# Optimization experiments

Hardware: AMD Instinct MI355X
Metric: run time of the kernel (lower is better)

Reference implementation:

```python
import jax, jax.numpy as jnp
import numpy as np

N = 50000   # nodes
E = 800000  # edges
F = 128     # feature dim per layer
BN_EPS = 1e-5


def setup_inputs() -> dict:
    key = jax.random.key(0)
    ks = jax.random.split(key, 4)
    x = jax.random.normal(ks[0], (N, F), dtype=jnp.float32)
    edge_index = jax.random.randint(ks[1], (2, E), 0, N, dtype=jnp.int64)
    scale = 1.0 / np.sqrt(F)
    W1 = jax.random.normal(ks[2], (F, F), dtype=jnp.float32) * scale
    W2 = jax.random.normal(ks[3], (F, F), dtype=jnp.float32) * scale
    zeros = jnp.zeros((F,), dtype=jnp.float32)
    ones = jnp.ones((F,), dtype=jnp.float32)
    prelu = jnp.full((1,), 0.25, dtype=jnp.float32)
    return {
        "x": x, "edge_index": edge_index,
        "W1": W1, "b1": zeros, "g1": ones, "be1": zeros, "a1": prelu,
        "W2": W2, "b2": zeros, "g2": ones, "be2": zeros, "a2": prelu,
    }


def _gcn_norm(edge_index):
    # PyG GCNConv: add self-loops, symmetric normalization D^-1/2 A D^-1/2
    src, dst = edge_index[0], edge_index[1]
    loop = jnp.arange(N, dtype=src.dtype)
    src_a = jnp.concatenate([src, loop])  # [E+N]
    dst_a = jnp.concatenate([dst, loop])
    w = jnp.ones((E + N,), dtype=jnp.float32)
    deg = jax.ops.segment_sum(w, dst_a, num_segments=N)
    dinv = jnp.where(deg > 0, jax.lax.rsqrt(jnp.maximum(deg, 1.0)), 0.0)
    norm = dinv[src_a] * w * dinv[dst_a]  # [E+N]
    return src_a, dst_a, norm


def _layer(x, src_a, dst_a, norm, W, b, g, be, a):
    h = x @ W                                    # [N,F] dense transform
    msg = h[src_a] * norm[:, None]               # gather [E+N,F]
    agg = jax.ops.segment_sum(msg, dst_a, num_segments=N) + b  # scatter-add
    # BatchNorm1d (training mode: biased batch statistics over nodes)
    mu = jnp.mean(agg, axis=0)
    var = jnp.mean(jnp.square(agg - mu), axis=0)
    xh = (agg - mu) * jax.lax.rsqrt(var + BN_EPS) * g + be
    # PReLU (single shared weight)
    return jnp.where(xh >= 0, xh, a * xh)


def reference(x, edge_index, W1, b1, g1, be1, a1, W2, b2, g2, be2, a2):
    src_a, dst_a, norm = _gcn_norm(edge_index)
    x = _layer(x, src_a, dst_a, norm, W1, b1, g1, be1, a1)
    x = _layer(x, src_a, dst_a, norm, W2, b2, g2, be2, a2)
    return x
```

## Files before the change

### kernel.cpp

```cpp
#include <hip/hip_runtime.h>

#define FD 128
#define BN_EPS 1e-5f
#define BSH 8
#define CAP 6144
#define BE 8192
#define NGB 2048
#define NRB 64

typedef short s8v __attribute__((ext_vector_type(8)));
typedef float f4v __attribute__((ext_vector_type(4)));

__device__ __forceinline__ unsigned short f2bf(float f) {
    unsigned u = __float_as_uint(f);
    u += 0x7fff + ((u >> 16) & 1);
    return (unsigned short)(u >> 16);
}
__device__ __forceinline__ float bf_lo(unsigned int u) {
    return __uint_as_float(u << 16);
}
__device__ __forceinline__ float bf_hi(unsigned int u) {
    return __uint_as_float(u & 0xffff0000u);
}

__global__ __launch_bounds__(256) void detect_kernel(const int* __restrict__ ei,
                                                     int n32, int* flag, int* gcur) {
    __shared__ int any;
    gcur[threadIdx.x] = 0;
    if (threadIdx.x == 0) any = 0;
    __syncthreads();
    int limit = n32 < 4096 ? n32 : 4096;
    int found = 0;
    for (int i = threadIdx.x * 2 + 1; i < limit; i += 512) {
        if (ei[i] != 0) { found = 1; break; }
    }
    if (found) atomicOr(&any, 1);
    __syncthreads();
    if (threadIdx.x == 0) flag[0] = any ? 0 : 1;
}

__device__ __forceinline__ int edge_get(const void* ei, int is64, size_t idx) {
    return is64 ? (int)((const long long*)ei)[idx] : ((const int*)ei)[idx];
}

__global__ __launch_bounds__(256) void partition_kernel(const void* ei, const int* flag,
                                                        int* __restrict__ gcur,
                                                        unsigned* __restrict__ slab, int E) {
    __shared__ int hist[256];
    __shared__ int base[256];
    __shared__ int cur[256];
    int t = threadIdx.x;
    int e0 = blockIdx.x * BE;
    int cnt = E - e0; if (cnt > BE) cnt = BE;
    hist[t] = 0;
    __syncthreads();
    int is64 = flag[0];
    for (int i = t; i < cnt; i += 256) {
        int d = edge_get(ei, is64, (size_t)E + e0 + i);
        atomicAdd(&hist[d >> BSH], 1);
    }
    __syncthreads();
    base[t] = hist[t] ? atomicAdd(&gcur[t], hist[t]) : 0;
    cur[t] = 0;
    __syncthreads();
    for (int i = t; i < cnt; i += 256) {
        int s = edge_get(ei, is64, e0 + i);
        int d = edge_get(ei, is64, (size_t)E + e0 + i);
        int b = d >> BSH;
        int r = atomicAdd(&cur[b], 1);
        int pos = base[b] + r;
        if (pos < CAP)
            slab[(size_t)b * CAP + pos] = (unsigned)s | ((unsigned)(d & 255) << 24);
    }
}

__global__ __launch_bounds__(256) void bucket_csr_kernel(const unsigned* __restrict__ slab,
                                                         const int* __restrict__ gcur,
                                                         int* __restrict__ colslab,
                                                         uint4* __restrict__ nodemeta,
                                                         float* __restrict__ dinv, int n) {
    __shared__ int hist[256];
    __shared__ int loc[256];
    __shared__ int cur[256];
    __shared__ int tmp[256];
    int b = blockIdx.x, t = threadIdx.x;
    hist[t] = 0;
    __syncthreads();
    int cnt = gcur[b]; if (cnt > CAP) cnt = CAP;
    const unsigned* sl = slab + (size_t)b * CAP;
    for (int i = t; i < cnt; i += 256)
        atomicAdd(&hist[sl[i] >> 24], 1);
    __syncthreads();
    int v = hist[t];
    tmp[t] = v;
    __syncthreads();
    for (int off = 1; off < 256; off <<= 1) {
        int x = (t >= off) ? tmp[t - off] : 0;
        __syncthreads();
        tmp[t] += x;
        __syncthreads();
    }
    int start_loc = tmp[t] - v;
    loc[t] = start_loc;
    cur[t] = 0;
    int node = (b << BSH) + t;
    if (node < n) {
        float dv = rsqrtf(1.0f + (float)v);
        dinv[node] = dv;
        nodemeta[node] = make_uint4((unsigned)(b * CAP + start_loc), (unsigned)v,
                                    __float_as_uint(dv), 0u);
    }
    __syncthreads();
    for (int i = t; i < cnt; i += 256) {
        unsigned e = sl[i];
        int dl = e >> 24;
        int r = atomicAdd(&cur[dl], 1);
        colslab[(size_t)b * CAP + loc[dl] + r] = (int)(e & 0xFFFFFF);
    }
}

__global__ __launch_bounds__(256) void wprep_kernel(const float* __restrict__ W1,
                                                    const float* __restrict__ W2,
                                                    unsigned short* __restrict__ Wf1,
                                                    unsigned short* __restrict__ Wf2) {
    int blk = blockIdx.x;
    const float* W = (blk < 64) ? W1 : W2;
    unsigned short* Wf = (blk < 64) ? Wf1 : Wf2;
    int idx = (blk & 63) * 256 + threadIdx.x;
    int j = idx & 7, lane = (idx >> 3) & 63, ct = (idx >> 9) & 7, kt = idx >> 12;
    int k = kt * 32 + (lane >> 4) * 8 + j;
    int c = ct * 16 + (lane & 15);
    Wf[idx] = f2bf(W[k * FD + c]);
}

template<int MODE>
__global__ __launch_bounds__(256) void gemm_mfma_kernel(const float* __restrict__ Ain,
                                                        const unsigned short* __restrict__ Wfrag,
                                                        const float* __restrict__ dinv,
                                                        const float4* __restrict__ scsh,
                                                        const float* __restrict__ aP,
                                                        unsigned short* __restrict__ C,
                                                        int n) {
    int wave = threadIdx.x >> 6, lane = threadIdx.x & 63;
    int rbase = blockIdx.x * 64 + wave * 16;
    int lrow = rbase + (lane & 15);
    int kg = lane >> 4;
    bool rok = lrow < n;
    float alpha = MODE ? aP[0] : 0.f;

    f4v acc[8];
#pragma unroll
    for (int i = 0; i < 8; ++i) acc[i] = (f4v){0.f, 0.f, 0.f, 0.f};

    const s8v* wf = (const s8v*)Wfrag;

#pragma unroll
    for (int kt = 0; kt < 4; ++kt) {
        s8v afr = (s8v){0, 0, 0, 0, 0, 0, 0, 0};
        if (rok) {
            const float* p = Ain + (size_t)lrow * FD + kt * 32 + kg * 8;
            float4 u0 = *(const float4*)p;
            float4 u1 = *(const float4*)(p + 4);
            if (MODE) {
                int c4 = kt * 8 + kg * 2;
                float4 sc0 = scsh[c4],      sh0 = scsh[32 + c4];
                float4 sc1 = scsh[c4 + 1],  sh1 = scsh[32 + c4 + 1];
                u0.x = u0.x * sc0.x + sh0.x; u0.y = u0.y * sc0.y + sh0.y;
                u0.z = u0.z * sc0.z + sh0.z; u0.w = u0.w * sc0.w + sh0.w;
                u1.x = u1.x * sc1.x + sh1.x; u1.y = u1.y * sc1.y + sh1.y;
                u1.z = u1.z * sc1.z + sh1.z; u1.w = u1.w * sc1.w + sh1.w;
                u0.x = u0.x >= 0.f ? u0.x : alpha * u0.x;
                u0.y = u0.y >= 0.f ? u0.y : alpha * u0.y;
                u0.z = u0.z >= 0.f ? u0.z : alpha * u0.z;
                u0.w = u0.w >= 0.f ? u0.w : alpha * u0.w;
                u1.x = u1.x >= 0.f ? u1.x : alpha * u1.x;
                u1.y = u1.y >= 0.f ? u1.y : alpha * u1.y;
                u1.z = u1.z >= 0.f ? u1.z : alpha * u1.z;
                u1.w = u1.w >= 0.f ? u1.w : alpha * u1.w;
            }
            afr[0] = (short)f2bf(u0.x); afr[1] = (short)f2bf(u0.y);
            afr[2] = (short)f2bf(u0.z); afr[3] = (short)f2bf(u0.w);
            afr[4] = (short)f2bf(u1.x); afr[5] = (short)f2bf(u1.y);
            afr[6] = (short)f2bf(u1.z); afr[7] = (short)f2bf(u1.w);
        }
#pragma unroll
        for (int ct = 0; ct < 8; ++ct) {
            s8v bfr = wf[(kt * 8 + ct) * 64 + lane];
            acc[ct] = __builtin_amdgcn_mfma_f32_16x16x32_bf16(afr, bfr, acc[ct], 0, 0, 0);
        }
    }

    int col0 = lane & 15;
#pragma unroll
    for (int r = 0; r < 4; ++r) {
        int row = rbase + kg * 4 + r;
        if (row < n) {
            float dv = dinv[row];
            unsigned short* crow = C + (size_t)row * FD;
#pragma unroll
            for (int ct = 0; ct < 8; ++ct)
                crow[ct * 16 + col0] = f2bf(acc[ct][r] * dv);
        }
    }
}

__global__ __launch_bounds__(256) void gather_stats_kernel(const uint2* __restrict__ hs2,
                                                           const uint4* __restrict__ nodemeta,
                                                           const int* __restrict__ col,
                                                           const float* __restrict__ b,
                                                           float4* __restrict__ agg4,
                                                           float4* __restrict__ partial,
                                                           int n) {
    __shared__ float4 redS[256];
    __shared__ float4 redQ[256];
    int tid = threadIdx.x;
    int hid = blockIdx.x * 8 + (tid >> 5);
    int q = tid & 31;
    float4 bb = ((const float4*)b)[q];

    float4 ssum = {0.f, 0.f, 0.f, 0.f};
    float4 ssq  = {0.f, 0.f, 0.f, 0.f};

    for (int wid = hid; wid < n; wid += NGB * 8) {
        uint4 m = nodemeta[wid];
        int i0 = (int)m.x, cnt = (int)m.y;
        float dv = __uint_as_float(m.z);
        uint2 u = hs2[(size_t)wid * 32 + q];
        float ax = bf_lo(u.x), ay = bf_hi(u.x), az = bf_lo(u.y), aw = bf_hi(u.y);
        int j = 0;
        for (; j + 4 <= cnt; j += 4) {
            int s0 = col[i0 + j], s1 = col[i0 + j + 1];
            int s2 = col[i0 + j + 2], s3 = col[i0 + j + 3];
            uint2 u0 = hs2[(size_t)s0 * 32 + q];
            uint2 u1 = hs2[(size_t)s1 * 32 + q];
            uint2 u2 = hs2[(size_t)s2 * 32 + q];
            uint2 u3 = hs2[(size_t)s3 * 32 + q];
            ax += bf_lo(u0.x) + bf_lo(u1.x) + bf_lo(u2.x) + bf_lo(u3.x);
            ay += bf_hi(u0.x) + bf_hi(u1.x) + bf_hi(u2.x) + bf_hi(u3.x);
            az += bf_lo(u0.y) + bf_lo(u1.y) + bf_lo(u2.y) + bf_lo(u3.y);
            aw += bf_hi(u0.y) + bf_hi(u1.y) + bf_hi(u2.y) + bf_hi(u3.y);
        }
        for (; j < cnt; ++j) {
            int s = col[i0 + j];
            uint2 uu = hs2[(size_t)s * 32 + q];
            ax += bf_lo(uu.x); ay += bf_hi(uu.x); az += bf_lo(uu.y); aw += bf_hi(uu.y);
        }
        float4 o;
        o.x = dv * ax + bb.x; o.y = dv * ay + bb.y;
        o.z = dv * az + bb.z; o.w = dv * aw + bb.w;
        agg4[(size_t)wid * 32 + q] = o;
        ssum.x += o.x; ssum.y += o.y; ssum.z += o.z; ssum.w += o.w;
        ssq.x += o.x * o.x; ssq.y += o.y * o.y;
        ssq.z += o.z * o.z; ssq.w += o.w * o.w;
    }
    redS[tid] = ssum;
    redQ[tid] = ssq;
    __syncthreads();
    if (tid < 128) {
        redS[tid].x += redS[tid+128].x; redS[tid].y += redS[tid+128].y;
        redS[tid].z += redS[tid+128].z; redS[tid].w += redS[tid+128].w;
        redQ[tid].x += redQ[tid+128].x; redQ[tid].y += redQ[tid+128].y;
        redQ[tid].z += redQ[tid+128].z; redQ[tid].w += redQ[tid+128].w;
    }
    __syncthreads();
    if (tid < 64) {
        redS[tid].x += redS[tid+64].x; redS[tid].y += redS[tid+64].y;
        redS[tid].z += redS[tid+64].z; redS[tid].w += redS[tid+64].w;
        redQ[tid].x += redQ[tid+64].x; redQ[tid].y += redQ[tid+64].y;
        redQ[tid].z += redQ[tid+64].z; redQ[tid].w += redQ[tid+64].w;
    }
    __syncthreads();
    if (tid < 32) {
        float4 s = redS[tid], s2 = redS[tid + 32];
        float4 qq = redQ[tid], q2 = redQ[tid + 32];
        s.x += s2.x; s.y += s2.y; s.z += s2.z; s.w += s2.w;
        qq.x += q2.x; qq.y += q2.y; qq.z += q2.z; qq.w += q2.w;
        partial[(size_t)blockIdx.x * 64 + tid] = s;
        partial[(size_t)blockIdx.x * 64 + 32 + tid] = qq;
    }
}

__global__ __launch_bounds__(256) void reduce_partial_kernel(const float4* __restrict__ partial,
                                                             float4* __restrict__ partial2) {
    __shared__ float4 red[256];
    int t = threadIdx.x;
    int e = t & 63;
    int sr = t >> 6;
    int r0 = blockIdx.x * 32;
    float4 acc = {0.f, 0.f, 0.f, 0.f};
    for (int r = sr; r < 32; r += 4) {
        float4 v = partial[(size_t)(r0 + r) * 64 + e];
        acc.x += v.x; acc.y += v.y; acc.z += v.z; acc.w += v.w;
    }
    red[t] = acc;
    __syncthreads();
    if (sr < 2) {
        float4 o = red[t + 128];
        red[t].x += o.x; red[t].y += o.y; red[t].z += o.z; red[t].w += o.w;
    }
    __syncthreads();
    if (sr == 0) {
        float4 o = red[t + 64];
        float4 s = red[t];
        s.x += o.x; s.y += o.y; s.z += o.z; s.w += o.w;
        partial2[(size_t)blockIdx.x * 64 + e] = s;
    }
}

__global__ __launch_bounds__(1024) void bn_finalize_kernel(const float4* __restrict__ partial2,
                                                           const float* __restrict__ g,
                                                           const float* __restrict__ be,
                                                           float4* __restrict__ scsh,
                                                           float invn) {
    __shared__ float4 red[1024];
    int t = threadIdx.x;
    int e = t & 63;
    int rg = t >> 6;
    float4 acc = {0.f, 0.f, 0.f, 0.f};
    for (int r = rg; r < NRB; r += 16) {
        float4 v = partial2[(size_t)r * 64 + e];
        acc.x += v.x; acc.y += v.y; acc.z += v.z; acc.w += v.w;
    }
    red[t] = acc;
    __syncthreads();
#pragma unroll
    for (int s = 8; s >= 1; s >>= 1) {
        if (rg < s) {
            float4 o = red[t + s * 64];
            red[t].x += o.x; red[t].y += o.y; red[t].z += o.z; red[t].w += o.w;
        }
        __syncthreads();
    }
    if (t < 32) {
        float4 s = red[t];
        float4 qq = red[32 + t];
        float4 gg = ((const float4*)g)[t];
        float4 bbe = ((const float4*)be)[t];
        float4 mu, var, sc, sh;
        mu.x = s.x * invn; mu.y = s.y * invn; mu.z = s.z * invn; mu.w = s.w * invn;
        var.x = qq.x * invn - mu.x * mu.x; var.y = qq.y * invn - mu.y * mu.y;
        var.z = qq.z * invn - mu.z * mu.z; var.w = qq.w * invn - mu.w * mu.w;
        sc.x = gg.x * rsqrtf(var.x + BN_EPS); sc.y = gg.y * rsqrtf(var.y + BN_EPS);
        sc.z = gg.z * rsqrtf(var.z + BN_EPS); sc.w = gg.w * rsqrtf(var.w + BN_EPS);
        sh.x = bbe.x - mu.x * sc.x; sh.y = bbe.y - mu.y * sc.y;
        sh.z = bbe.z - mu.z * sc.z; sh.w = bbe.w - mu.w * sc.w;
        scsh[t] = sc;
        scsh[32 + t] = sh;
    }
}

__global__ __launch_bounds__(256) void bn_apply_kernel(const float4* __restrict__ agg4,
                                                       const float4* __restrict__ scsh,
                                                       const float* __restrict__ aP,
                                                       float4* __restrict__ out, int n) {
    int t = blockIdx.x * 256 + threadIdx.x;
    if (t >= n * 32) return;
    int c4 = t & 31;
    float alpha = aP[0];
    float4 v = agg4[t];
    float4 sc = scsh[c4];
    float4 sh = scsh[32 + c4];
    float4 y;
    y.x = v.x * sc.x + sh.x; y.y = v.y * sc.y + sh.y;
    y.z = v.z * sc.z + sh.z; y.w = v.w * sc.w + sh.w;
    y.x = y.x >= 0.f ? y.x : alpha * y.x;
    y.y = y.y >= 0.f ? y.y : alpha * y.y;
    y.z = y.z >= 0.f ? y.z : alpha * y.z;
    y.w = y.w >= 0.f ? y.w : alpha * y.w;
    out[t] = y;
}


extern "C" void kernel_launch(void* const* d_in, const int* in_sizes, int n_in,
                              void* d_out, int out_size, void* d_ws, size_t ws_size,
                              hipStream_t stream) {
    const float* x  = (const float*)d_in[0];
    const void*  ei = d_in[1];
    const float* W1 = (const float*)d_in[2];
    const float* b1 = (const float*)d_in[3];
    const float* g1 = (const float*)d_in[4];
    const float* be1= (const float*)d_in[5];
    const float* a1 = (const float*)d_in[6];
    const float* W2 = (const float*)d_in[7];
    const float* b2 = (const float*)d_in[8];
    const float* g2 = (const float*)d_in[9];
    const float* be2= (const float*)d_in[10];
    const float* a2 = (const float*)d_in[11];

    int N = in_sizes[0] / FD;
    int E = in_sizes[1] / 2;
    float* out = (float*)d_out;

    int nbuck = (N + (1 << BSH) - 1) >> BSH;

    char* ws = (char*)d_ws;
    size_t off = 0;
    auto alloc = [&](size_t bytes) {
        void* p = ws + off;
        off += (bytes + 255) & ~(size_t)255;
        return p;
    };
    float* dinv    = (float*)alloc((size_t)N * 4);
    int*   flag    = (int*)alloc(256);
    int*   gcur    = (int*)alloc(256 * 4);
    uint4* nodemeta= (uint4*)alloc((size_t)N * 16);
    unsigned* slab = (unsigned*)alloc((size_t)nbuck * CAP * 4);
    int*   colslab = (int*)alloc((size_t)nbuck * CAP * 4);
    unsigned short* wf1 = (unsigned short*)alloc((size_t)FD * FD * 2);
    unsigned short* wf2 = (unsigned short*)alloc((size_t)FD * FD * 2);
    unsigned short* hs  = (unsigned short*)alloc((size_t)N * FD * 2);
    float4* agg    = (float4*)alloc((size_t)N * FD * 4);
    float4* partial= (float4*)alloc((size_t)NGB * 64 * 16);
    float4* partial2=(float4*)alloc((size_t)NRB * 64 * 16);
    float4* scsh   = (float4*)alloc(64 * 16);
    (void)ws_size; (void)n_in; (void)out_size;

    detect_kernel<<<1, 256, 0, stream>>>((const int*)ei, 2 * E, flag, gcur);

    partition_kernel<<<(E + BE - 1) / BE, 256, 0, stream>>>(ei, flag, gcur, slab, E);
    bucket_csr_kernel<<<nbuck, 256, 0, stream>>>(slab, gcur, colslab, nodemeta, dinv, N);

    wprep_kernel<<<128, 256, 0, stream>>>(W1, W2, wf1, wf2);

    int gemm_blocks = (N + 63) / 64;
    int nt = N * 32;
    float invn = 1.0f / (float)N;

    gemm_mfma_kernel<0><<<gemm_blocks, 256, 0, stream>>>(x, wf1, dinv, nullptr, nullptr,
                                                         hs, N);
    gather_stats_kernel<<<NGB, 256, 0, stream>>>((const uint2*)hs, nodemeta, colslab,
                                                 b1, agg, partial, N);
    reduce_partial_kernel<<<NRB, 256, 0, stream>>>(partial, partial2);
    bn_finalize_kernel<<<1, 1024, 0, stream>>>(partial2, g1, be1, scsh, invn);

    gemm_mfma_kernel<1><<<gemm_blocks, 256, 0, stream>>>((const float*)agg, wf2, dinv,
                                                         scsh, a1, hs, N);
    gather_stats_kernel<<<NGB, 256, 0, stream>>>((const uint2*)hs, nodemeta, colslab,
                                                 b2, agg, partial, N);
    reduce_partial_kernel<<<NRB, 256, 0, stream>>>(partial, partial2);
    bn_finalize_kernel<<<1, 1024, 0, stream>>>(partial2, g2, be2, scsh, invn);
    bn_apply_kernel<<<(nt + 255) / 256, 256, 0, stream>>>(agg, scsh, a2, (float4*)out, N);
}
```

Measured before the change: 167.0 us.

## Store aggregated features in bf16 and fold int64 detection into partition

The aggregation buffer is now written as packed bf16 instead of fp32, which halves the traffic for the gather write, the second GEMM's read and the final BN-apply read. The separate detect kernel is removed. Each partition block now checks the index width itself, and the counters are cleared with a memset. In exchange, the pre-BN aggregate loses precision before the second layer's normalization and the final output, and the dtype check is repeated in every partition block.

```diff
diff --git a/kernel.cpp b/kernel.cpp
--- a/kernel.cpp
+++ b/kernel.cpp
@@ -16,45 +16,46 @@
     u += 0x7fff + ((u >> 16) & 1);
     return (unsigned short)(u >> 16);
 }
+__device__ __forceinline__ unsigned pack2(float a, float b) {
+    return (unsigned)f2bf(a) | ((unsigned)f2bf(b) << 16);
+}
 __device__ __forceinline__ float bf_lo(unsigned int u) {
     return __uint_as_float(u << 16);
 }
 __device__ __forceinline__ float bf_hi(unsigned int u) {
     return __uint_as_float(u & 0xffff0000u);
 }
-
-__global__ __launch_bounds__(256) void detect_kernel(const int* __restrict__ ei,
-                                                     int n32, int* flag, int* gcur) {
-    __shared__ int any;
-    gcur[threadIdx.x] = 0;
-    if (threadIdx.x == 0) any = 0;
-    __syncthreads();
-    int limit = n32 < 4096 ? n32 : 4096;
-    int found = 0;
-    for (int i = threadIdx.x * 2 + 1; i < limit; i += 512) {
-        if (ei[i] != 0) { found = 1; break; }
-    }
-    if (found) atomicOr(&any, 1);
-    __syncthreads();
-    if (threadIdx.x == 0) flag[0] = any ? 0 : 1;
+__device__ __forceinline__ float bfu(unsigned short s) {
+    return __uint_as_float(((unsigned)s) << 16);
 }
 
 __device__ __forceinline__ int edge_get(const void* ei, int is64, size_t idx) {
     return is64 ? (int)((const long long*)ei)[idx] : ((const int*)ei)[idx];
 }
 
-__global__ __launch_bounds__(256) void partition_kernel(const void* ei, const int* flag,
+__global__ __launch_bounds__(256) void partition_kernel(const void* ei,
                                                         int* __restrict__ gcur,
                                                         unsigned* __restrict__ slab, int E) {
+    __shared__ int any;
     __shared__ int hist[256];
     __shared__ int base[256];
     __shared__ int cur[256];
     int t = threadIdx.x;
+    if (t == 0) any = 0;
+    hist[t] = 0;
+    __syncthreads();
+    {
+        const int* e32 = (const int*)ei;
+        int limit = 2 * E < 4096 ? 2 * E : 4096;
+        int found = 0;
+        for (int i = t * 2 + 1; i < limit; i += 512)
+            if (e32[i] != 0) { found = 1; break; }
+        if (found) atomicOr(&any, 1);
+    }
+    __syncthreads();
+    int is64 = any ? 0 : 1;
     int e0 = blockIdx.x * BE;
     int cnt = E - e0; if (cnt > BE) cnt = BE;
-    hist[t] = 0;
-    __syncthreads();
-    int is64 = flag[0];
     for (int i = t; i < cnt; i += 256) {
         int d = edge_get(ei, is64, (size_t)E + e0 + i);
         atomicAdd(&hist[d >> BSH], 1);
@@ -134,7 +135,7 @@
 }
 
 template<int MODE>
-__global__ __launch_bounds__(256) void gemm_mfma_kernel(const float* __restrict__ Ain,
+__global__ __launch_bounds__(256) void gemm_mfma_kernel(const void* __restrict__ Ain,
                                                         const unsigned short* __restrict__ Wfrag,
                                                         const float* __restrict__ dinv,
                                                         const float4* __restrict__ scsh,
@@ -158,10 +159,14 @@
     for (int kt = 0; kt < 4; ++kt) {
         s8v afr = (s8v){0, 0, 0, 0, 0, 0, 0, 0};
         if (rok) {
-            const float* p = Ain + (size_t)lrow * FD + kt * 32 + kg * 8;
-            float4 u0 = *(const float4*)p;
-            float4 u1 = *(const float4*)(p + 4);
+            float4 u0, u1;
             if (MODE) {
+                const unsigned short* A = (const unsigned short*)Ain;
+                s8v raw = *(const s8v*)(A + (size_t)lrow * FD + kt * 32 + kg * 8);
+                u0.x = bfu((unsigned short)raw[0]); u0.y = bfu((unsigned short)raw[1]);
+                u0.z = bfu((unsigned short)raw[2]); u0.w = bfu((unsigned short)raw[3]);
+                u1.x = bfu((unsigned short)raw[4]); u1.y = bfu((unsigned short)raw[5]);
+                u1.z = bfu((unsigned short)raw[6]); u1.w = bfu((unsigned short)raw[7]);
                 int c4 = kt * 8 + kg * 2;
                 float4 sc0 = scsh[c4],      sh0 = scsh[32 + c4];
                 float4 sc1 = scsh[c4 + 1],  sh1 = scsh[32 + c4 + 1];
@@ -177,6 +182,11 @@
                 u1.y = u1.y >= 0.f ? u1.y : alpha * u1.y;
                 u1.z = u1.z >= 0.f ? u1.z : alpha * u1.z;
                 u1.w = u1.w >= 0.f ? u1.w : alpha * u1.w;
+            } else {
+                const float* A = (const float*)Ain;
+                const float* p = A + (size_t)lrow * FD + kt * 32 + kg * 8;
+                u0 = *(const float4*)p;
+                u1 = *(const float4*)(p + 4);
             }
             afr[0] = (short)f2bf(u0.x); afr[1] = (short)f2bf(u0.y);
             afr[2] = (short)f2bf(u0.z); afr[3] = (short)f2bf(u0.w);
@@ -208,7 +218,7 @@
                                                            const uint4* __restrict__ nodemeta,
                                                            const int* __restrict__ col,
                                                            const float* __restrict__ b,
-                                                           float4* __restrict__ agg4,
+                                                           uint2* __restrict__ aggb,
                                                            float4* __restrict__ partial,
                                                            int n) {
     __shared__ float4 redS[256];
@@ -248,7 +258,10 @@
         float4 o;
         o.x = dv * ax + bb.x; o.y = dv * ay + bb.y;
         o.z = dv * az + bb.z; o.w = dv * aw + bb.w;
-        agg4[(size_t)wid * 32 + q] = o;
+        uint2 w;
+        w.x = pack2(o.x, o.y);
+        w.y = pack2(o.z, o.w);
+        aggb[(size_t)wid * 32 + q] = w;
         ssum.x += o.x; ssum.y += o.y; ssum.z += o.z; ssum.w += o.w;
         ssq.x += o.x * o.x; ssq.y += o.y * o.y;
         ssq.z += o.z * o.z; ssq.w += o.w * o.w;
@@ -349,7 +362,7 @@
     }
 }
 
-__global__ __launch_bounds__(256) void bn_apply_kernel(const float4* __restrict__ agg4,
+__global__ __launch_bounds__(256) void bn_apply_kernel(const uint2* __restrict__ aggb,
                                                        const float4* __restrict__ scsh,
                                                        const float* __restrict__ aP,
                                                        float4* __restrict__ out, int n) {
@@ -357,7 +370,9 @@
     if (t >= n * 32) return;
     int c4 = t & 31;
     float alpha = aP[0];
-    float4 v = agg4[t];
+    uint2 u = aggb[t];
+    float4 v;
+    v.x = bf_lo(u.x); v.y = bf_hi(u.x); v.z = bf_lo(u.y); v.w = bf_hi(u.y);
     float4 sc = scsh[c4];
     float4 sh = scsh[32 + c4];
     float4 y;
@@ -401,7 +416,6 @@
         return p;
     };
     float* dinv    = (float*)alloc((size_t)N * 4);
-    int*   flag    = (int*)alloc(256);
     int*   gcur    = (int*)alloc(256 * 4);
     uint4* nodemeta= (uint4*)alloc((size_t)N * 16);
     unsigned* slab = (unsigned*)alloc((size_t)nbuck * CAP * 4);
@@ -409,15 +423,15 @@
     unsigned short* wf1 = (unsigned short*)alloc((size_t)FD * FD * 2);
     unsigned short* wf2 = (unsigned short*)alloc((size_t)FD * FD * 2);
     unsigned short* hs  = (unsigned short*)alloc((size_t)N * FD * 2);
-    float4* agg    = (float4*)alloc((size_t)N * FD * 4);
+    uint2* aggb    = (uint2*)alloc((size_t)N * FD * 2);
     float4* partial= (float4*)alloc((size_t)NGB * 64 * 16);
     float4* partial2=(float4*)alloc((size_t)NRB * 64 * 16);
     float4* scsh   = (float4*)alloc(64 * 16);
     (void)ws_size; (void)n_in; (void)out_size;
 
-    detect_kernel<<<1, 256, 0, stream>>>((const int*)ei, 2 * E, flag, gcur);
-
-    partition_kernel<<<(E + BE - 1) / BE, 256, 0, stream>>>(ei, flag, gcur, slab, E);
+    hipMemsetAsync(gcur, 0, 256 * 4, stream);
+
+    partition_kernel<<<(E + BE - 1) / BE, 256, 0, stream>>>(ei, gcur, slab, E);
     bucket_csr_kernel<<<nbuck, 256, 0, stream>>>(slab, gcur, colslab, nodemeta, dinv, N);
 
     wprep_kernel<<<128, 256, 0, stream>>>(W1, W2, wf1, wf2);
@@ -429,15 +443,15 @@
     gemm_mfma_kernel<0><<<gemm_blocks, 256, 0, stream>>>(x, wf1, dinv, nullptr, nullptr,
                                                          hs, N);
     gather_stats_kernel<<<NGB, 256, 0, stream>>>((const uint2*)hs, nodemeta, colslab,
-                                                 b1, agg, partial, N);
+                                                 b1, aggb, partial, N);
     reduce_partial_kernel<<<NRB, 256, 0, stream>>>(partial, partial2);
     bn_finalize_kernel<<<1, 1024, 0, stream>>>(partial2, g1, be1, scsh, invn);
 
-    gemm_mfma_kernel<1><<<gemm_blocks, 256, 0, stream>>>((const float*)agg, wf2, dinv,
+    gemm_mfma_kernel<1><<<gemm_blocks, 256, 0, stream>>>(aggb, wf2, dinv,
                                                          scsh, a1, hs, N);
     gather_stats_kernel<<<NGB, 256, 0, stream>>>((const uint2*)hs, nodemeta, colslab,
-                                                 b2, agg, partial, N);
+                                                 b2, aggb, partial, N);
     reduce_partial_kernel<<<NRB, 256, 0, stream>>>(partial, partial2);
     bn_finalize_kernel<<<1, 1024, 0, stream>>>(partial2, g2, be2, scsh, invn);
-    bn_apply_kernel<<<(nt + 255) / 256, 256, 0, stream>>>(agg, scsh, a2, (float4*)out, N);
-}
+    bn_apply_kernel<<<(nt + 255) / 256, 256, 0, stream>>>(aggb, scsh, a2, (float4*)out, N);
+}
```

Measured after the change: 165.2 us. About the same (-1.1%).
